# Optimization experiments

Measured on AMD Instinct MI355X. Metric: run time of the kernel, lower is better.

The kernel has to match this reference:

```python
import jax, jax.numpy as jnp
import numpy as np

B = 512              # number of graphs
NODES_PER_G = 256    # equal-size graphs (required by jagged reshape in original)
N = B * NODES_PER_G  # total nodes
DEG = 16
E = N * DEG
F = 16               # num_node_features (coords + 2-dim selected encoding)
D = 64               # embedding_dim
H = 128              # hidden_output_dim
A = 1                # actions_output_dim
MAX_LV = 3


def setup_inputs() -> dict:
    key = jax.random.key(0)
    ks = jax.random.split(key, 12)
    node_features = jax.random.normal(ks[0], (N, F), dtype=jnp.float32)
    # edges restricted to within each graph, fixed out-degree DEG
    edge_dst = jnp.repeat(jnp.arange(N, dtype=jnp.int32), DEG)
    base = (edge_dst // NODES_PER_G) * NODES_PER_G
    edge_src = base + jax.random.randint(ks[1], (E,), 0, NODES_PER_G, dtype=jnp.int32)
    seg_ids = (jnp.arange(N, dtype=jnp.int32) // NODES_PER_G)
    forbidden_mask = jax.random.bernoulli(ks[2], 0.1, (N,))
    s = 1.0 / np.sqrt(F)
    Wn = jax.random.uniform(ks[3], (F, D), jnp.float32, -s, s)
    bn = jax.random.uniform(ks[4], (D,), jnp.float32, -s, s)
    s = 1.0 / np.sqrt(D)
    Wc = jax.random.uniform(ks[5], (D, D), jnp.float32, -s, s)
    bc = jax.random.uniform(ks[6], (D,), jnp.float32, -s, s)
    s = 1.0 / np.sqrt(2 * D)
    W1 = jax.random.uniform(ks[7], (2 * D, H), jnp.float32, -s, s)
    b1 = jax.random.uniform(ks[8], (H,), jnp.float32, -s, s)
    s = 1.0 / np.sqrt(H)
    W2 = jax.random.uniform(ks[9], (H, A), jnp.float32, -s, s)
    b2 = jax.random.uniform(ks[10], (A,), jnp.float32, -s, s)
    return {"node_features": node_features, "edge_src": edge_src, "edge_dst": edge_dst,
            "seg_ids": seg_ids, "forbidden_mask": forbidden_mask,
            "Wn": Wn, "bn": bn, "Wc": Wc, "bc": bc,
            "W1": W1, "b1": b1, "W2": W2, "b2": b2}


def reference(node_features, edge_src, edge_dst, seg_ids, forbidden_mask,
              Wn, bn, Wc, bc, W1, b1, W2, b2):
    # --- structure2vec mean-field (EmbedMeanField, output_dim=0, max_lv=3) ---
    input_msg = node_features @ Wn + bn            # [N, D]
    h = jax.nn.relu(input_msg)
    for _ in range(MAX_LV):
        pooled = jax.ops.segment_sum(h[edge_src], edge_dst, num_segments=N)  # adjacency spmm
        h = jax.nn.relu(pooled @ Wc + bc + input_msg)
    graph_embed = jax.nn.relu(jax.ops.segment_sum(h, seg_ids, num_segments=B))  # [B, D]
    # --- actions is None: repeat graph embed per node, concat, small MLP ---
    rep = graph_embed[seg_ids]                     # rep_global_embed
    embed_s_a = jnp.concatenate([h, rep], axis=1)  # [N, 2D]
    raw_pred = jax.nn.relu(embed_s_a @ W1 + b1) @ W2 + b2  # [N, A]
    # --- greedy action select with forbidden-action masking + jagged topk ---
    q = raw_pred.reshape(-1)                       # A == 1
    q = jnp.where(forbidden_mask, jnp.float32(np.finfo(np.float32).min), q)
    jag = q.reshape(B, NODES_PER_G)
    values = jnp.max(jag, axis=1, keepdims=True)
    indices = jnp.argmax(jag, axis=1, keepdims=True)
    return indices, raw_pred, values
```

## Files before the change

### kernel.cpp

```cpp
#include <hip/hip_runtime.h>

#define NB 512
#define NPG 256
#define NTOT (NB * NPG)
#define NEGMIN -3.4028234663852886e38f

#define OFF_WNT 0
#define OFF_WCT 1024
#define OFF_W1AT 5120
#define OFF_W1BT 13312
#define OFF_BNC 21504
#define WS_FLOATS 21568

__global__ __launch_bounds__(256) void prep_kernel(
    const float* __restrict__ Wn, const float* __restrict__ bn,
    const float* __restrict__ Wc, const float* __restrict__ bc,
    const float* __restrict__ W1, float* __restrict__ ws)
{
    int i = blockIdx.x * 256 + threadIdx.x;
    if (i < 1024) {
        int d = i >> 4, k = i & 15;
        ws[OFF_WNT + i] = Wn[k * 64 + d];
    } else if (i < 5120) {
        int j = i - 1024; int d = j >> 6, k = j & 63;
        ws[OFF_WCT + j] = Wc[k * 64 + d];
    } else if (i < 13312) {
        int j = i - 5120; int r = j >> 6, k = j & 63;
        ws[OFF_W1AT + j] = W1[k * 128 + r];
    } else if (i < 21504) {
        int j = i - 13312; int r = j >> 6, k = j & 63;
        ws[OFF_W1BT + j] = W1[(64 + k) * 128 + r];
    } else if (i < WS_FLOATS) {
        int d = i - OFF_BNC;
        ws[OFF_BNC + d] = bn[d] + bc[d];
    }
}

__global__ __launch_bounds__(256, 2) void gdqn_kernel(
    const float* __restrict__ nfg, const int* __restrict__ esrcg,
    const int* __restrict__ fmask, const float* __restrict__ ws,
    const float* __restrict__ bn, const float* __restrict__ b1,
    const float* __restrict__ W2, const float* __restrict__ b2,
    float* __restrict__ out)
{
    extern __shared__ float smem[];
    float* hsh  = smem;
    float* part = smem + 16384;
    float* gesh = smem + 16640;
    float* rpsh = smem + 16704;
    float* redv = smem + 16832;
    int*   redi = (int*)(smem + 16836);

    const int g = blockIdx.x, t = threadIdx.x;
    const int node = (g << 8) + t;
    const int swt = t & 7;
    float* myrow = hsh + (t << 6);

    const float* WnT  = ws + OFF_WNT;
    const float* WcT  = ws + OFF_WCT;
    const float* W1aT = ws + OFF_W1AT;
    const float* bnc  = ws + OFF_BNC;

    float nf[16];
    {
        const float4* p = (const float4*)(nfg + node * 16);
        float4 a = p[0], b = p[1], c = p[2], d = p[3];
        nf[0]=a.x; nf[1]=a.y; nf[2]=a.z; nf[3]=a.w;
        nf[4]=b.x; nf[5]=b.y; nf[6]=b.z; nf[7]=b.w;
        nf[8]=c.x; nf[9]=c.y; nf[10]=c.z; nf[11]=c.w;
        nf[12]=d.x; nf[13]=d.y; nf[14]=d.z; nf[15]=d.w;
    }
    int es[16];
    {
        const int4* p = (const int4*)(esrcg + node * 16);
        int4 a = p[0], b = p[1], c = p[2], d = p[3];
        es[0]=a.x&255; es[1]=a.y&255; es[2]=a.z&255; es[3]=a.w&255;
        es[4]=b.x&255; es[5]=b.y&255; es[6]=b.z&255; es[7]=b.w&255;
        es[8]=c.x&255; es[9]=c.y&255; es[10]=c.z&255; es[11]=c.w&255;
        es[12]=d.x&255; es[13]=d.y&255; es[14]=d.z&255; es[15]=d.w&255;
    }

    for (int c = 0; c < 16; ++c) {
        float s4[4];
        #pragma unroll
        for (int q = 0; q < 4; ++q) {
            int d = 4 * c + q;
            float s = bn[d];
            #pragma unroll
            for (int k = 0; k < 16; ++k) s = fmaf(nf[k], WnT[d * 16 + k], s);
            s4[q] = fmaxf(s, 0.0f);
        }
        ((float4*)myrow)[c ^ swt] = make_float4(s4[0], s4[1], s4[2], s4[3]);
    }
    __syncthreads();

    for (int lv = 0; lv < 3; ++lv) {
        float pooled[64];
        #pragma unroll
        for (int k = 0; k < 64; ++k) pooled[k] = 0.0f;
        #pragma unroll
        for (int j = 0; j < 16; ++j) {
            int s = es[j];
            const float4* row = (const float4*)(hsh + (s << 6));
            int sw = s & 7;
            #pragma unroll
            for (int c = 0; c < 16; ++c) {
                float4 v = row[c ^ sw];
                pooled[4*c+0] += v.x; pooled[4*c+1] += v.y;
                pooled[4*c+2] += v.z; pooled[4*c+3] += v.w;
            }
        }
        __syncthreads();

        for (int c = 0; c < 16; ++c) {
            float s4[4];
            #pragma unroll
            for (int q = 0; q < 4; ++q) {
                int d = 4 * c + q;
                float s = bnc[d];
                #pragma unroll
                for (int k = 0; k < 16; ++k) s = fmaf(nf[k], WnT[d * 16 + k], s);
                const float* wr = WcT + d * 64;
                #pragma unroll
                for (int k = 0; k < 64; ++k) s = fmaf(pooled[k], wr[k], s);
                s4[q] = fmaxf(s, 0.0f);
            }
            ((float4*)myrow)[c ^ swt] = make_float4(s4[0], s4[1], s4[2], s4[3]);
        }
        __syncthreads();
    }

    {
        int col = t & 63, v0 = (t >> 6) << 6;
        float s = 0.0f;
        for (int v = 0; v < 64; ++v) {
            int vv = v0 + v;
            s += hsh[(vv << 6) + ((((col >> 2) ^ (vv & 7)) << 2) | (col & 3))];
        }
        part[t] = s;
    }
    __syncthreads();
    if (t < 64) {
        float s = part[t] + part[t + 64] + part[t + 128] + part[t + 192];
        gesh[t] = fmaxf(s, 0.0f);
    }
    __syncthreads();
    if (t < 128) {
        float s = b1[t];
        const float4* wr = (const float4*)(ws + OFF_W1BT + t * 64);
        #pragma unroll
        for (int c = 0; c < 16; ++c) {
            float4 w = wr[c];
            s = fmaf(gesh[4*c+0], w.x, s);
            s = fmaf(gesh[4*c+1], w.y, s);
            s = fmaf(gesh[4*c+2], w.z, s);
            s = fmaf(gesh[4*c+3], w.w, s);
        }
        rpsh[t] = s;
    }

    float h[64];
    #pragma unroll
    for (int c = 0; c < 16; ++c) {
        float4 v = ((const float4*)myrow)[c ^ swt];
        h[4*c+0] = v.x; h[4*c+1] = v.y; h[4*c+2] = v.z; h[4*c+3] = v.w;
    }
    __syncthreads();

    float raw = b2[0];
    for (int j = 0; j < 128; ++j) {
        float z = rpsh[j];
        const float* wr = W1aT + j * 64;
        #pragma unroll
        for (int k = 0; k < 64; ++k) z = fmaf(h[k], wr[k], z);
        raw = fmaf(fmaxf(z, 0.0f), W2[j], raw);
    }
    out[512 + node] = raw;

    float q = fmask[node] ? NEGMIN : raw;
    int idx = t;
    #pragma unroll
    for (int off = 32; off >= 1; off >>= 1) {
        float ov = __shfl_down(q, off, 64);
        int oi  = __shfl_down(idx, off, 64);
        if (ov > q || (ov == q && oi < idx)) { q = ov; idx = oi; }
    }
    if ((t & 63) == 0) { redv[t >> 6] = q; redi[t >> 6] = idx; }
    __syncthreads();
    if (t == 0) {
        float bv = redv[0]; int bi = redi[0];
        #pragma unroll
        for (int w = 1; w < 4; ++w) {
            float v = redv[w]; int iw = redi[w];
            if (v > bv || (v == bv && iw < bi)) { bv = v; bi = iw; }
        }
        out[g] = (float)bi;
        out[512 + NTOT + g] = bv;
    }
}

extern "C" void kernel_launch(void* const* d_in, const int* in_sizes, int n_in,
                              void* d_out, int out_size, void* d_ws, size_t ws_size,
                              hipStream_t stream)
{
    const float* nfg   = (const float*)d_in[0];
    const int*   esrc  = (const int*)d_in[1];
    const int*   fmask = (const int*)d_in[4];
    const float* Wn = (const float*)d_in[5];
    const float* bn = (const float*)d_in[6];
    const float* Wc = (const float*)d_in[7];
    const float* bc = (const float*)d_in[8];
    const float* W1 = (const float*)d_in[9];
    const float* b1 = (const float*)d_in[10];
    const float* W2 = (const float*)d_in[11];
    const float* b2 = (const float*)d_in[12];
    float* out = (float*)d_out;
    float* ws  = (float*)d_ws;

    prep_kernel<<<(WS_FLOATS + 255) / 256, 256, 0, stream>>>(Wn, bn, Wc, bc, W1, ws);

    size_t shmem = 16840 * sizeof(float);
    hipFuncSetAttribute((const void*)gdqn_kernel,
                        hipFuncAttributeMaxDynamicSharedMemorySize, (int)shmem);
    gdqn_kernel<<<NB, 256, shmem, stream>>>(nfg, esrc, fmask, ws, bn, b1, W2, b2, out);
}
```

Before: 260.0 us.

## Split each node's embedding dims across two threads with padded LDS rows

Raises the block to 512 threads so that each node is handled by two threads, each owning 32 of the 64 embedding dimensions for gathering and for the Wc matmul. Partial pooled halves are exchanged through shared memory, which costs extra barriers per level, and the XOR-swizzled row layout is replaced by rows padded to 68 floats. The aim is more parallel work per graph and lower per-thread register pressure for better latency hiding. The final MLP still runs on only half the threads, leaving the other 256 idle during that phase.

```diff
diff --git a/kernel.cpp b/kernel.cpp
--- a/kernel.cpp
+++ b/kernel.cpp
@@ -3,6 +3,7 @@
 #define NB 512
 #define NPG 256
 #define NTOT (NB * NPG)
+#define RS 68
 #define NEGMIN -3.4028234663852886e38f
 
 #define OFF_WNT 0
@@ -36,7 +37,7 @@
     }
 }
 
-__global__ __launch_bounds__(256, 2) void gdqn_kernel(
+__global__ __launch_bounds__(512, 4) void gdqn_kernel(
     const float* __restrict__ nfg, const int* __restrict__ esrcg,
     const int* __restrict__ fmask, const float* __restrict__ ws,
     const float* __restrict__ bn, const float* __restrict__ b1,
@@ -45,21 +46,25 @@
 {
     extern __shared__ float smem[];
     float* hsh  = smem;
-    float* part = smem + 16384;
-    float* gesh = smem + 16640;
-    float* rpsh = smem + 16704;
-    float* redv = smem + 16832;
-    int*   redi = (int*)(smem + 16836);
-
-    const int g = blockIdx.x, t = threadIdx.x;
-    const int node = (g << 8) + t;
-    const int swt = t & 7;
-    float* myrow = hsh + (t << 6);
+    float* part = smem + 17408;
+    float* gesh = smem + 17920;
+    float* rpsh = smem + 17984;
+    float* redv = smem + 18112;
+    int*   redi = (int*)(smem + 18116);
+
+    const int g = blockIdx.x, tid = threadIdx.x;
+    const int n = tid & 255;
+    const int u = tid >> 8;
+    const int d0 = u << 5;
+    const int node = (g << 8) + n;
 
     const float* WnT  = ws + OFF_WNT;
     const float* WcT  = ws + OFF_WCT;
     const float* W1aT = ws + OFF_W1AT;
     const float* bnc  = ws + OFF_BNC;
+
+    float* myrow  = hsh + n * RS;
+    float* myhalf = myrow + d0;
 
     float nf[16];
     {
@@ -80,74 +85,82 @@
         es[12]=d.x&255; es[13]=d.y&255; es[14]=d.z&255; es[15]=d.w&255;
     }
 
-    for (int c = 0; c < 16; ++c) {
+    for (int cc = 0; cc < 8; ++cc) {
         float s4[4];
         #pragma unroll
         for (int q = 0; q < 4; ++q) {
-            int d = 4 * c + q;
+            int d = d0 + 4 * cc + q;
             float s = bn[d];
             #pragma unroll
             for (int k = 0; k < 16; ++k) s = fmaf(nf[k], WnT[d * 16 + k], s);
             s4[q] = fmaxf(s, 0.0f);
         }
-        ((float4*)myrow)[c ^ swt] = make_float4(s4[0], s4[1], s4[2], s4[3]);
+        ((float4*)myhalf)[cc] = make_float4(s4[0], s4[1], s4[2], s4[3]);
     }
     __syncthreads();
 
     for (int lv = 0; lv < 3; ++lv) {
-        float pooled[64];
-        #pragma unroll
-        for (int k = 0; k < 64; ++k) pooled[k] = 0.0f;
+        float pooled[32];
+        #pragma unroll
+        for (int k = 0; k < 32; ++k) pooled[k] = 0.0f;
         #pragma unroll
         for (int j = 0; j < 16; ++j) {
-            int s = es[j];
-            const float4* row = (const float4*)(hsh + (s << 6));
-            int sw = s & 7;
-            #pragma unroll
-            for (int c = 0; c < 16; ++c) {
-                float4 v = row[c ^ sw];
-                pooled[4*c+0] += v.x; pooled[4*c+1] += v.y;
-                pooled[4*c+2] += v.z; pooled[4*c+3] += v.w;
+            const float4* row = (const float4*)(hsh + es[j] * RS + d0);
+            #pragma unroll
+            for (int cc = 0; cc < 8; ++cc) {
+                float4 v = row[cc];
+                pooled[4*cc+0] += v.x; pooled[4*cc+1] += v.y;
+                pooled[4*cc+2] += v.z; pooled[4*cc+3] += v.w;
             }
         }
         __syncthreads();
 
+        #pragma unroll
+        for (int cc = 0; cc < 8; ++cc)
+            ((float4*)myhalf)[cc] = make_float4(pooled[4*cc], pooled[4*cc+1],
+                                                pooled[4*cc+2], pooled[4*cc+3]);
+        __syncthreads();
+        float pf[64];
+        #pragma unroll
         for (int c = 0; c < 16; ++c) {
+            float4 v = ((const float4*)myrow)[c];
+            pf[4*c+0] = v.x; pf[4*c+1] = v.y; pf[4*c+2] = v.z; pf[4*c+3] = v.w;
+        }
+        __syncthreads();
+
+        for (int cc = 0; cc < 8; ++cc) {
             float s4[4];
             #pragma unroll
             for (int q = 0; q < 4; ++q) {
-                int d = 4 * c + q;
+                int d = d0 + 4 * cc + q;
                 float s = bnc[d];
                 #pragma unroll
                 for (int k = 0; k < 16; ++k) s = fmaf(nf[k], WnT[d * 16 + k], s);
                 const float* wr = WcT + d * 64;
                 #pragma unroll
-                for (int k = 0; k < 64; ++k) s = fmaf(pooled[k], wr[k], s);
+                for (int k = 0; k < 64; ++k) s = fmaf(pf[k], wr[k], s);
                 s4[q] = fmaxf(s, 0.0f);
             }
-            ((float4*)myrow)[c ^ swt] = make_float4(s4[0], s4[1], s4[2], s4[3]);
-        }
-        __syncthreads();
-    }
-
-    {
-        int col = t & 63, v0 = (t >> 6) << 6;
+            ((float4*)myhalf)[cc] = make_float4(s4[0], s4[1], s4[2], s4[3]);
+        }
+        __syncthreads();
+    }
+
+    if (tid < 256) {
+        int col = tid & 63, v0 = (tid >> 6) << 6;
         float s = 0.0f;
-        for (int v = 0; v < 64; ++v) {
-            int vv = v0 + v;
-            s += hsh[(vv << 6) + ((((col >> 2) ^ (vv & 7)) << 2) | (col & 3))];
-        }
-        part[t] = s;
-    }
-    __syncthreads();
-    if (t < 64) {
-        float s = part[t] + part[t + 64] + part[t + 128] + part[t + 192];
-        gesh[t] = fmaxf(s, 0.0f);
-    }
-    __syncthreads();
-    if (t < 128) {
-        float s = b1[t];
-        const float4* wr = (const float4*)(ws + OFF_W1BT + t * 64);
+        for (int v = 0; v < 64; ++v) s += hsh[(v0 + v) * RS + col];
+        part[tid] = s;
+    }
+    __syncthreads();
+    if (tid < 64) {
+        float s = part[tid] + part[tid + 64] + part[tid + 128] + part[tid + 192];
+        gesh[tid] = fmaxf(s, 0.0f);
+    }
+    __syncthreads();
+    if (tid < 128) {
+        float s = b1[tid];
+        const float4* wr = (const float4*)(ws + OFF_W1BT + tid * 64);
         #pragma unroll
         for (int c = 0; c < 16; ++c) {
             float4 w = wr[c];
@@ -156,38 +169,42 @@
             s = fmaf(gesh[4*c+2], w.z, s);
             s = fmaf(gesh[4*c+3], w.w, s);
         }
-        rpsh[t] = s;
+        rpsh[tid] = s;
     }
 
     float h[64];
     #pragma unroll
     for (int c = 0; c < 16; ++c) {
-        float4 v = ((const float4*)myrow)[c ^ swt];
+        float4 v = ((const float4*)myrow)[c];
         h[4*c+0] = v.x; h[4*c+1] = v.y; h[4*c+2] = v.z; h[4*c+3] = v.w;
     }
     __syncthreads();
 
-    float raw = b2[0];
-    for (int j = 0; j < 128; ++j) {
-        float z = rpsh[j];
-        const float* wr = W1aT + j * 64;
-        #pragma unroll
-        for (int k = 0; k < 64; ++k) z = fmaf(h[k], wr[k], z);
-        raw = fmaf(fmaxf(z, 0.0f), W2[j], raw);
-    }
-    out[512 + node] = raw;
-
-    float q = fmask[node] ? NEGMIN : raw;
-    int idx = t;
+    float raw = 0.0f;
+    if (tid < 256) {
+        raw = b2[0];
+        for (int j = 0; j < 128; ++j) {
+            float z = rpsh[j];
+            const float* wr = W1aT + j * 64;
+            #pragma unroll
+            for (int k = 0; k < 64; ++k) z = fmaf(h[k], wr[k], z);
+            raw = fmaf(fmaxf(z, 0.0f), W2[j], raw);
+        }
+        out[512 + node] = raw;
+    }
+
+    float q = NEGMIN;
+    if (tid < 256) q = fmask[node] ? NEGMIN : raw;
+    int idx = n;
     #pragma unroll
     for (int off = 32; off >= 1; off >>= 1) {
         float ov = __shfl_down(q, off, 64);
         int oi  = __shfl_down(idx, off, 64);
         if (ov > q || (ov == q && oi < idx)) { q = ov; idx = oi; }
     }
-    if ((t & 63) == 0) { redv[t >> 6] = q; redi[t >> 6] = idx; }
-    __syncthreads();
-    if (t == 0) {
+    if (tid < 256 && (tid & 63) == 0) { redv[tid >> 6] = q; redi[tid >> 6] = idx; }
+    __syncthreads();
+    if (tid == 0) {
         float bv = redv[0]; int bi = redi[0];
         #pragma unroll
         for (int w = 1; w < 4; ++w) {
@@ -219,8 +236,8 @@
 
     prep_kernel<<<(WS_FLOATS + 255) / 256, 256, 0, stream>>>(Wn, bn, Wc, bc, W1, ws);
 
-    size_t shmem = 16840 * sizeof(float);
+    size_t shmem = 18120 * sizeof(float);
     hipFuncSetAttribute((const void*)gdqn_kernel,
                         hipFuncAttributeMaxDynamicSharedMemorySize, (int)shmem);
-    gdqn_kernel<<<NB, 256, shmem, stream>>>(nfg, esrc, fmask, ws, bn, b1, W2, b2, out);
+    gdqn_kernel<<<NB, 512, shmem, stream>>>(nfg, esrc, fmask, ws, bn, b1, W2, b2, out);
 }
```

Result: slower. 371.3 us (+42.8%).
